# Performance work log

Hardware: AMD Instinct MI355X
Metric: run time of the kernel (lower is better)

## Reference

```python
import jax, jax.numpy as jnp
import numpy as np

IN_F = (16, 16, 16)
OUT_F = (16, 16, 16)
RANKS = (8, 8, 8, 8, 8, 8)


def setup_inputs() -> dict:
    key = jax.random.key(0)
    ks = jax.random.split(key, 9)
    x = jax.random.normal(ks[0], (4096, int(np.prod(IN_F))), dtype=jnp.float32)
    # core ~ U[0,1)*0.1 as in torch.rand(ranks)*0.1
    core = jax.random.uniform(ks[1], RANKS, dtype=jnp.float32) * 0.1
    # factor matrices: 3 out-side (out_f[i], r[i]) then 3 in-side (in_f[i], r[i+3])
    shapes = [(OUT_F[i], RANKS[i]) for i in range(3)] + [(IN_F[i], RANKS[i + 3]) for i in range(3)]
    f0, f1, f2, f3, f4, f5 = [
        jax.random.normal(ks[2 + i], shapes[i], dtype=jnp.float32) * 0.1 for i in range(6)
    ]
    bias = jnp.zeros((int(np.prod(OUT_F)),), dtype=jnp.float32)
    return {"x": x, "core": core, "f0": f0, "f1": f1, "f2": f2,
            "f3": f3, "f4": f4, "f5": f5, "bias": bias}


def reference(x, core, f0, f1, f2, f3, f4, f5, bias):
    # x: [N, prod(IN_F)] -> [N, i1, i2, i3]
    xr = x.reshape(-1, *IN_F)
    # Reconstruct full dense weight from Tucker factors (faithful to original)
    # core: [r0..r5]; f0..f2 out-side (out_dim, r); f3..f5 in-side (in_dim, r)
    W = jnp.einsum('ijklmn,ai,bj,ck,dl,em,fn->abcdef', core, f0, f1, f2, f3, f4, f5)
    # Contract input with in-side modes: [N, o1, o2, o3]
    res = jnp.einsum('abcdef,ndef->nabc', W, xr)
    y = res.reshape(-1, int(np.prod(OUT_F)))
    return y + bias
```

## Files before the change

### kernel.cpp

```cpp
#include <hip/hip_runtime.h>

#define THREADS 256

typedef __attribute__((ext_vector_type(8))) short bf16x8;
typedef __attribute__((ext_vector_type(4))) float f32x4;

__device__ inline unsigned short f2bf(float f) {
    union { float f; unsigned int u; } v; v.f = f;
    unsigned int r = v.u + 0x7fffu + ((v.u >> 16) & 1u);
    return (unsigned short)(r >> 16);
}

__global__ __launch_bounds__(THREADS) void k_in_contract(
    const float* __restrict__ x,
    const float* __restrict__ f3, const float* __restrict__ f4,
    const float* __restrict__ f5,
    unsigned short* __restrict__ u3b, int N)
{
    const int n = blockIdx.x;
    const int t = threadIdx.x;

    __shared__ float fs[256];
    __shared__ float u1s[256 * 9];
    __shared__ float u2s[128 * 9];

    if (t < 128) { fs[t] = f3[t]; fs[128 + t] = f4[t]; }

    float xv[16];
    {
        const float4* xr = (const float4*)(x + (size_t)n * 4096 + t * 16);
        float4 a0 = xr[0], a1 = xr[1], a2 = xr[2], a3 = xr[3];
        xv[0]=a0.x; xv[1]=a0.y; xv[2]=a0.z; xv[3]=a0.w;
        xv[4]=a1.x; xv[5]=a1.y; xv[6]=a1.z; xv[7]=a1.w;
        xv[8]=a2.x; xv[9]=a2.y; xv[10]=a2.z; xv[11]=a2.w;
        xv[12]=a3.x; xv[13]=a3.y; xv[14]=a3.z; xv[15]=a3.w;
    }

    float acc8[8];
    #pragma unroll
    for (int q = 0; q < 8; ++q) acc8[q] = 0.f;
    #pragma unroll
    for (int f = 0; f < 16; ++f) {
        const float xf = xv[f];
        #pragma unroll
        for (int n6 = 0; n6 < 8; ++n6)
            acc8[n6] = fmaf(xf, f5[f*8 + n6], acc8[n6]);
    }
    __syncthreads();
    #pragma unroll
    for (int n6 = 0; n6 < 8; ++n6) u1s[t*9 + n6] = acc8[n6];
    __syncthreads();

    {
        const int d = t >> 4, m = (t >> 1) & 7, h = t & 1;
        float fr[16];
        #pragma unroll
        for (int e = 0; e < 16; ++e) fr[e] = fs[128 + e*8 + m];
        float a4[4] = {0.f, 0.f, 0.f, 0.f};
        #pragma unroll
        for (int e = 0; e < 16; ++e) {
            const int base = (d*16 + e)*9 + h*4;
            #pragma unroll
            for (int q = 0; q < 4; ++q)
                a4[q] = fmaf(u1s[base + q], fr[e], a4[q]);
        }
        #pragma unroll
        for (int q = 0; q < 4; ++q) u2s[(d*8 + m)*9 + h*4 + q] = a4[q];
    }
    __syncthreads();

    {
        const int l = t >> 5, m = (t >> 2) & 7, h = t & 3;
        float fr[16];
        #pragma unroll
        for (int d = 0; d < 16; ++d) fr[d] = fs[d*8 + l];
        float a2[2] = {0.f, 0.f};
        #pragma unroll
        for (int d = 0; d < 16; ++d) {
            const int base = (d*8 + m)*9 + h*2;
            a2[0] = fmaf(u2s[base],     fr[d], a2[0]);
            a2[1] = fmaf(u2s[base + 1], fr[d], a2[1]);
        }
        unsigned int pk = (unsigned int)f2bf(a2[0]) |
                          ((unsigned int)f2bf(a2[1]) << 16);
        ((unsigned int*)u3b)[(size_t)n * 256 + t] = pk;
    }
}

__global__ __launch_bounds__(THREADS) void k_convert_core(
    const float* __restrict__ core, unsigned short* __restrict__ coreb)
{
    const int i = blockIdx.x * THREADS + threadIdx.x;
    float4 c = ((const float4*)core)[i];
    ushort4 o;
    o.x = f2bf(c.x); o.y = f2bf(c.y); o.z = f2bf(c.z); o.w = f2bf(c.w);
    ((ushort4*)coreb)[i] = o;
}

__global__ __launch_bounds__(THREADS) void k_core_gemm_mfma(
    const unsigned short* __restrict__ u3b,
    const unsigned short* __restrict__ coreb,
    float* __restrict__ v, int N)
{
    const int t    = threadIdx.x;
    const int lane = t & 63;
    const int wave = t >> 6;
    const int m0 = blockIdx.x * 128 + wave * 32;
    const int p0 = blockIdx.y * 32;
    const int lr = lane & 15;
    const int lq = lane >> 4;

    const unsigned short* aptr0 = u3b   + (size_t)(m0 + lr) * 512 + lq * 8;
    const unsigned short* aptr1 = aptr0 + 16 * 512;
    const unsigned short* bptr0 = coreb + (size_t)(p0 + lr) * 512 + lq * 8;
    const unsigned short* bptr1 = bptr0 + 16 * 512;

    f32x4 acc00 = {0.f,0.f,0.f,0.f}, acc01 = {0.f,0.f,0.f,0.f};
    f32x4 acc10 = {0.f,0.f,0.f,0.f}, acc11 = {0.f,0.f,0.f,0.f};

    #pragma unroll
    for (int k0 = 0; k0 < 512; k0 += 32) {
        bf16x8 a0 = *(const bf16x8*)(aptr0 + k0);
        bf16x8 a1 = *(const bf16x8*)(aptr1 + k0);
        bf16x8 b0 = *(const bf16x8*)(bptr0 + k0);
        bf16x8 b1 = *(const bf16x8*)(bptr1 + k0);
        acc00 = __builtin_amdgcn_mfma_f32_16x16x32_bf16(a0, b0, acc00, 0, 0, 0);
        acc01 = __builtin_amdgcn_mfma_f32_16x16x32_bf16(a0, b1, acc01, 0, 0, 0);
        acc10 = __builtin_amdgcn_mfma_f32_16x16x32_bf16(a1, b0, acc10, 0, 0, 0);
        acc11 = __builtin_amdgcn_mfma_f32_16x16x32_bf16(a1, b1, acc11, 0, 0, 0);
    }

    const int row = m0 + lq * 4;
    const int col = p0 + lr;
    #pragma unroll
    for (int r = 0; r < 4; ++r) {
        v[(size_t)(row + r) * 512 + col]           = acc00[r];
        v[(size_t)(row + r) * 512 + col + 16]      = acc01[r];
        v[(size_t)(row + 16 + r) * 512 + col]      = acc10[r];
        v[(size_t)(row + 16 + r) * 512 + col + 16] = acc11[r];
    }
}

__global__ __launch_bounds__(THREADS) void k_out_expand(
    const float* __restrict__ v,
    const float* __restrict__ f0, const float* __restrict__ f1,
    const float* __restrict__ f2, const float* __restrict__ bias,
    float* __restrict__ y, int N)
{
    const int n = blockIdx.x;
    const int t = threadIdx.x;

    __shared__ float fs[256];
    __shared__ float vs[512];
    __shared__ float w1s[128 * 9];
    __shared__ float w2s[256 * 9];

    if (t < 128) { fs[t] = f0[t]; fs[128 + t] = f1[t]; }
    if (t < 128) ((float4*)vs)[t] = ((const float4*)(v + (size_t)n*512))[t];
    __syncthreads();

    {
        const int a = t >> 4, j = (t >> 1) & 7, h = t & 1;
        float fr[8];
        #pragma unroll
        for (int i = 0; i < 8; ++i) fr[i] = fs[a*8 + i];
        float a4[4] = {0.f, 0.f, 0.f, 0.f};
        #pragma unroll
        for (int i = 0; i < 8; ++i) {
            const int base = i*64 + j*8 + h*4;
            #pragma unroll
            for (int q = 0; q < 4; ++q)
                a4[q] = fmaf(vs[base + q], fr[i], a4[q]);
        }
        #pragma unroll
        for (int q = 0; q < 4; ++q) w1s[(a*8 + j)*9 + h*4 + q] = a4[q];
    }
    __syncthreads();

    {
        const int a = t >> 4, b = t & 15;
        float fr[8];
        #pragma unroll
        for (int j = 0; j < 8; ++j) fr[j] = fs[128 + b*8 + j];
        float a8[8] = {0.f,0.f,0.f,0.f,0.f,0.f,0.f,0.f};
        #pragma unroll
        for (int j = 0; j < 8; ++j) {
            const int base = (a*8 + j)*9;
            const float fj = fr[j];
            #pragma unroll
            for (int k = 0; k < 8; ++k)
                a8[k] = fmaf(w1s[base + k], fj, a8[k]);
        }
        #pragma unroll
        for (int k = 0; k < 8; ++k) w2s[(a*16 + b)*9 + k] = a8[k];
    }
    __syncthreads();

    {
        const int a = t >> 4, b = t & 15;
        float wr[8];
        #pragma unroll
        for (int k = 0; k < 8; ++k) wr[k] = w2s[(a*16 + b)*9 + k];

        const int obase = a*256 + b*16;
        float4 b4[4];
        {
            const float4* bp = (const float4*)(bias + obase);
            b4[0] = bp[0]; b4[1] = bp[1]; b4[2] = bp[2]; b4[3] = bp[3];
        }
        float yv[16];
        #pragma unroll
        for (int q = 0; q < 4; ++q) {
            yv[q*4+0] = b4[q].x; yv[q*4+1] = b4[q].y;
            yv[q*4+2] = b4[q].z; yv[q*4+3] = b4[q].w;
        }
        #pragma unroll
        for (int c = 0; c < 16; ++c) {
            float s = yv[c];
            #pragma unroll
            for (int k = 0; k < 8; ++k)
                s = fmaf(wr[k], f2[c*8 + k], s);
            yv[c] = s;
        }
        float4* o = (float4*)(y + (size_t)n*4096 + obase);
        #pragma unroll
        for (int q = 0; q < 4; ++q)
            o[q] = make_float4(yv[q*4+0], yv[q*4+1], yv[q*4+2], yv[q*4+3]);
    }
}

extern "C" void kernel_launch(void* const* d_in, const int* in_sizes, int n_in,
                              void* d_out, int out_size, void* d_ws, size_t ws_size,
                              hipStream_t stream)
{
    const float* x    = (const float*)d_in[0];
    const float* core = (const float*)d_in[1];
    const float* f0   = (const float*)d_in[2];
    const float* f1   = (const float*)d_in[3];
    const float* f2   = (const float*)d_in[4];
    const float* f3   = (const float*)d_in[5];
    const float* f4   = (const float*)d_in[6];
    const float* f5   = (const float*)d_in[7];
    const float* bias = (const float*)d_in[8];
    float* y = (float*)d_out;

    const int N = in_sizes[0] / 4096;

    unsigned short* u3b   = (unsigned short*)d_ws;
    unsigned short* coreb = u3b + (size_t)N * 512;
    float*          v     = (float*)(coreb + 512 * 512);

    k_in_contract<<<N, THREADS, 0, stream>>>(x, f3, f4, f5, u3b, N);
    k_convert_core<<<256, THREADS, 0, stream>>>(core, coreb);
    dim3 gb(N / 128, 512 / 32);
    k_core_gemm_mfma<<<gb, THREADS, 0, stream>>>(u3b, coreb, v, N);
    k_out_expand<<<N, THREADS, 0, stream>>>(v, f0, f1, f2, bias, y, N);
}
```

Baseline: 163.5 us.

## Fuse core GEMM with output expansion and fold core conversion into input contraction

Cuts the pipeline from four launches to two. The core bf16 conversion moves into the input-contraction kernel, which now handles two rows per block. The MFMA core GEMM is fused with the three output-side factor contractions, so each block computes 8 rows of v in shared memory and expands them directly to y. This drops the v round-trip through global memory and two launches. In exchange, the fused GEMM uses only 8 of the 16 MFMA rows and each block rereads the whole core matrix, and intermediates are now stored as bf16, which lowers precision.

```diff
diff --git a/kernel.cpp b/kernel.cpp
--- a/kernel.cpp
+++ b/kernel.cpp
@@ -10,45 +10,69 @@
     unsigned int r = v.u + 0x7fffu + ((v.u >> 16) & 1u);
     return (unsigned short)(r >> 16);
 }
-
-__global__ __launch_bounds__(THREADS) void k_in_contract(
+__device__ inline unsigned int pack2(float lo, float hi) {
+    return (unsigned int)f2bf(lo) | ((unsigned int)f2bf(hi) << 16);
+}
+__device__ inline float bflo(unsigned int u) {
+    union { unsigned int u; float f; } v; v.u = u << 16; return v.f;
+}
+__device__ inline float bfhi(unsigned int u) {
+    union { unsigned int u; float f; } v; v.u = u & 0xffff0000u; return v.f;
+}
+
+__global__ __launch_bounds__(THREADS) void k_in_contract2(
     const float* __restrict__ x,
     const float* __restrict__ f3, const float* __restrict__ f4,
-    const float* __restrict__ f5,
-    unsigned short* __restrict__ u3b, int N)
+    const float* __restrict__ f5, const float* __restrict__ core,
+    unsigned short* __restrict__ u3b, unsigned short* __restrict__ coreb,
+    int N)
 {
-    const int n = blockIdx.x;
-    const int t = threadIdx.x;
+    const int n0 = blockIdx.x * 2;
+    const int t  = threadIdx.x;
 
     __shared__ float fs[256];
-    __shared__ float u1s[256 * 9];
-    __shared__ float u2s[128 * 9];
+    __shared__ float u1s[2][256 * 9];
+    __shared__ float u2s[2][128 * 9];
 
     if (t < 128) { fs[t] = f3[t]; fs[128 + t] = f4[t]; }
 
-    float xv[16];
-    {
-        const float4* xr = (const float4*)(x + (size_t)n * 4096 + t * 16);
+    if (blockIdx.x < 256) {
+        const int i = blockIdx.x * THREADS + t;
+        float4 c = ((const float4*)core)[i];
+        ushort4 o;
+        o.x = f2bf(c.x); o.y = f2bf(c.y); o.z = f2bf(c.z); o.w = f2bf(c.w);
+        ((ushort4*)coreb)[i] = o;
+    }
+
+    float xv[2][16];
+    #pragma unroll
+    for (int rr = 0; rr < 2; ++rr) {
+        const float4* xr = (const float4*)(x + (size_t)(n0 + rr) * 4096 + t * 16);
         float4 a0 = xr[0], a1 = xr[1], a2 = xr[2], a3 = xr[3];
-        xv[0]=a0.x; xv[1]=a0.y; xv[2]=a0.z; xv[3]=a0.w;
-        xv[4]=a1.x; xv[5]=a1.y; xv[6]=a1.z; xv[7]=a1.w;
-        xv[8]=a2.x; xv[9]=a2.y; xv[10]=a2.z; xv[11]=a2.w;
-        xv[12]=a3.x; xv[13]=a3.y; xv[14]=a3.z; xv[15]=a3.w;
-    }
-
-    float acc8[8];
-    #pragma unroll
-    for (int q = 0; q < 8; ++q) acc8[q] = 0.f;
+        xv[rr][0]=a0.x;  xv[rr][1]=a0.y;  xv[rr][2]=a0.z;  xv[rr][3]=a0.w;
+        xv[rr][4]=a1.x;  xv[rr][5]=a1.y;  xv[rr][6]=a1.z;  xv[rr][7]=a1.w;
+        xv[rr][8]=a2.x;  xv[rr][9]=a2.y;  xv[rr][10]=a2.z; xv[rr][11]=a2.w;
+        xv[rr][12]=a3.x; xv[rr][13]=a3.y; xv[rr][14]=a3.z; xv[rr][15]=a3.w;
+    }
+
+    float acc8[2][8];
+    #pragma unroll
+    for (int q = 0; q < 8; ++q) { acc8[0][q] = 0.f; acc8[1][q] = 0.f; }
     #pragma unroll
     for (int f = 0; f < 16; ++f) {
-        const float xf = xv[f];
-        #pragma unroll
-        for (int n6 = 0; n6 < 8; ++n6)
-            acc8[n6] = fmaf(xf, f5[f*8 + n6], acc8[n6]);
-    }
-    __syncthreads();
-    #pragma unroll
-    for (int n6 = 0; n6 < 8; ++n6) u1s[t*9 + n6] = acc8[n6];
+        #pragma unroll
+        for (int n6 = 0; n6 < 8; ++n6) {
+            const float w = f5[f*8 + n6];
+            acc8[0][n6] = fmaf(xv[0][f], w, acc8[0][n6]);
+            acc8[1][n6] = fmaf(xv[1][f], w, acc8[1][n6]);
+        }
+    }
+    __syncthreads();
+    #pragma unroll
+    for (int n6 = 0; n6 < 8; ++n6) {
+        u1s[0][t*9 + n6] = acc8[0][n6];
+        u1s[1][t*9 + n6] = acc8[1][n6];
+    }
     __syncthreads();
 
     {
@@ -56,16 +80,21 @@
         float fr[16];
         #pragma unroll
         for (int e = 0; e < 16; ++e) fr[e] = fs[128 + e*8 + m];
-        float a4[4] = {0.f, 0.f, 0.f, 0.f};
+        float a4[2][4] = {};
         #pragma unroll
         for (int e = 0; e < 16; ++e) {
             const int base = (d*16 + e)*9 + h*4;
             #pragma unroll
-            for (int q = 0; q < 4; ++q)
-                a4[q] = fmaf(u1s[base + q], fr[e], a4[q]);
-        }
-        #pragma unroll
-        for (int q = 0; q < 4; ++q) u2s[(d*8 + m)*9 + h*4 + q] = a4[q];
+            for (int q = 0; q < 4; ++q) {
+                a4[0][q] = fmaf(u1s[0][base + q], fr[e], a4[0][q]);
+                a4[1][q] = fmaf(u1s[1][base + q], fr[e], a4[1][q]);
+            }
+        }
+        #pragma unroll
+        for (int q = 0; q < 4; ++q) {
+            u2s[0][(d*8 + m)*9 + h*4 + q] = a4[0][q];
+            u2s[1][(d*8 + m)*9 + h*4 + q] = a4[1][q];
+        }
     }
     __syncthreads();
 
@@ -74,158 +103,154 @@
         float fr[16];
         #pragma unroll
         for (int d = 0; d < 16; ++d) fr[d] = fs[d*8 + l];
-        float a2[2] = {0.f, 0.f};
+        float a2[2][2] = {};
         #pragma unroll
         for (int d = 0; d < 16; ++d) {
             const int base = (d*8 + m)*9 + h*2;
-            a2[0] = fmaf(u2s[base],     fr[d], a2[0]);
-            a2[1] = fmaf(u2s[base + 1], fr[d], a2[1]);
-        }
-        unsigned int pk = (unsigned int)f2bf(a2[0]) |
-                          ((unsigned int)f2bf(a2[1]) << 16);
-        ((unsigned int*)u3b)[(size_t)n * 256 + t] = pk;
-    }
-}
-
-__global__ __launch_bounds__(THREADS) void k_convert_core(
-    const float* __restrict__ core, unsigned short* __restrict__ coreb)
-{
-    const int i = blockIdx.x * THREADS + threadIdx.x;
-    float4 c = ((const float4*)core)[i];
-    ushort4 o;
-    o.x = f2bf(c.x); o.y = f2bf(c.y); o.z = f2bf(c.z); o.w = f2bf(c.w);
-    ((ushort4*)coreb)[i] = o;
-}
-
-__global__ __launch_bounds__(THREADS) void k_core_gemm_mfma(
+            a2[0][0] = fmaf(u2s[0][base],     fr[d], a2[0][0]);
+            a2[0][1] = fmaf(u2s[0][base + 1], fr[d], a2[0][1]);
+            a2[1][0] = fmaf(u2s[1][base],     fr[d], a2[1][0]);
+            a2[1][1] = fmaf(u2s[1][base + 1], fr[d], a2[1][1]);
+        }
+        ((unsigned int*)u3b)[(size_t)(n0+0) * 256 + t] = pack2(a2[0][0], a2[0][1]);
+        ((unsigned int*)u3b)[(size_t)(n0+1) * 256 + t] = pack2(a2[1][0], a2[1][1]);
+    }
+}
+
+__global__ __launch_bounds__(THREADS) void k_gemm_expand(
     const unsigned short* __restrict__ u3b,
     const unsigned short* __restrict__ coreb,
-    float* __restrict__ v, int N)
-{
-    const int t    = threadIdx.x;
-    const int lane = t & 63;
-    const int wave = t >> 6;
-    const int m0 = blockIdx.x * 128 + wave * 32;
-    const int p0 = blockIdx.y * 32;
-    const int lr = lane & 15;
-    const int lq = lane >> 4;
-
-    const unsigned short* aptr0 = u3b   + (size_t)(m0 + lr) * 512 + lq * 8;
-    const unsigned short* aptr1 = aptr0 + 16 * 512;
-    const unsigned short* bptr0 = coreb + (size_t)(p0 + lr) * 512 + lq * 8;
-    const unsigned short* bptr1 = bptr0 + 16 * 512;
-
-    f32x4 acc00 = {0.f,0.f,0.f,0.f}, acc01 = {0.f,0.f,0.f,0.f};
-    f32x4 acc10 = {0.f,0.f,0.f,0.f}, acc11 = {0.f,0.f,0.f,0.f};
-
-    #pragma unroll
-    for (int k0 = 0; k0 < 512; k0 += 32) {
-        bf16x8 a0 = *(const bf16x8*)(aptr0 + k0);
-        bf16x8 a1 = *(const bf16x8*)(aptr1 + k0);
-        bf16x8 b0 = *(const bf16x8*)(bptr0 + k0);
-        bf16x8 b1 = *(const bf16x8*)(bptr1 + k0);
-        acc00 = __builtin_amdgcn_mfma_f32_16x16x32_bf16(a0, b0, acc00, 0, 0, 0);
-        acc01 = __builtin_amdgcn_mfma_f32_16x16x32_bf16(a0, b1, acc01, 0, 0, 0);
-        acc10 = __builtin_amdgcn_mfma_f32_16x16x32_bf16(a1, b0, acc10, 0, 0, 0);
-        acc11 = __builtin_amdgcn_mfma_f32_16x16x32_bf16(a1, b1, acc11, 0, 0, 0);
-    }
-
-    const int row = m0 + lq * 4;
-    const int col = p0 + lr;
-    #pragma unroll
-    for (int r = 0; r < 4; ++r) {
-        v[(size_t)(row + r) * 512 + col]           = acc00[r];
-        v[(size_t)(row + r) * 512 + col + 16]      = acc01[r];
-        v[(size_t)(row + 16 + r) * 512 + col]      = acc10[r];
-        v[(size_t)(row + 16 + r) * 512 + col + 16] = acc11[r];
-    }
-}
-
-__global__ __launch_bounds__(THREADS) void k_out_expand(
-    const float* __restrict__ v,
     const float* __restrict__ f0, const float* __restrict__ f1,
     const float* __restrict__ f2, const float* __restrict__ bias,
     float* __restrict__ y, int N)
 {
-    const int n = blockIdx.x;
-    const int t = threadIdx.x;
-
-    __shared__ float fs[256];
-    __shared__ float vs[512];
-    __shared__ float w1s[128 * 9];
-    __shared__ float w2s[256 * 9];
-
-    if (t < 128) { fs[t] = f0[t]; fs[128 + t] = f1[t]; }
-    if (t < 128) ((float4*)vs)[t] = ((const float4*)(v + (size_t)n*512))[t];
-    __syncthreads();
-
-    {
-        const int a = t >> 4, j = (t >> 1) & 7, h = t & 1;
-        float fr[8];
-        #pragma unroll
-        for (int i = 0; i < 8; ++i) fr[i] = fs[a*8 + i];
-        float a4[4] = {0.f, 0.f, 0.f, 0.f};
-        #pragma unroll
-        for (int i = 0; i < 8; ++i) {
-            const int base = i*64 + j*8 + h*4;
-            #pragma unroll
-            for (int q = 0; q < 4; ++q)
-                a4[q] = fmaf(vs[base + q], fr[i], a4[q]);
-        }
-        #pragma unroll
-        for (int q = 0; q < 4; ++q) w1s[(a*8 + j)*9 + h*4 + q] = a4[q];
-    }
-    __syncthreads();
-
-    {
-        const int a = t >> 4, b = t & 15;
-        float fr[8];
-        #pragma unroll
-        for (int j = 0; j < 8; ++j) fr[j] = fs[128 + b*8 + j];
-        float a8[8] = {0.f,0.f,0.f,0.f,0.f,0.f,0.f,0.f};
+    __shared__ float        vsS[8 * 520];
+    __shared__ unsigned int w1S[8 * 528];
+    __shared__ unsigned int w2S[8 * 1300];
+    __shared__ float        fsS[256];
+
+    const int t  = threadIdx.x;
+    const int r0 = blockIdx.x * 8;
+
+    fsS[t] = (t < 128) ? f0[t] : f1[t - 128];
+
+    {
+        const int lane = t & 63, w = t >> 6;
+        const int lr = lane & 15, lq = lane >> 4;
+        const unsigned short* ap = u3b + (size_t)(r0 + (lr & 7)) * 512 + lq * 8;
+        const unsigned short* bp = coreb + (size_t)(w * 128 + lr) * 512 + lq * 8;
+
+        f32x4 acc[8];
+        #pragma unroll
+        for (int c = 0; c < 8; ++c) acc[c] = (f32x4){0.f, 0.f, 0.f, 0.f};
+
+        #pragma unroll
+        for (int k0 = 0; k0 < 512; k0 += 32) {
+            bf16x8 a = *(const bf16x8*)(ap + k0);
+            #pragma unroll
+            for (int c = 0; c < 8; ++c) {
+                bf16x8 b = *(const bf16x8*)(bp + c * 8192 + k0);
+                acc[c] = __builtin_amdgcn_mfma_f32_16x16x32_bf16(a, b, acc[c], 0, 0, 0);
+            }
+        }
+        if (lq < 2) {
+            #pragma unroll
+            for (int c = 0; c < 8; ++c)
+                #pragma unroll
+                for (int q = 0; q < 4; ++q)
+                    vsS[(lq*4 + q)*520 + w*128 + c*16 + lr] = acc[c][q];
+        }
+    }
+    __syncthreads();
+
+    {
+        const int r = t >> 5, a = (t >> 1) & 15, h = t & 1;
+        const float* vrow = vsS + r*520 + h*32;
+        float fa[8];
+        #pragma unroll
+        for (int i = 0; i < 8; ++i) fa[i] = fsS[a*8 + i];
+        #pragma unroll
+        for (int q2 = 0; q2 < 16; ++q2) {
+            float s0 = 0.f, s1 = 0.f;
+            #pragma unroll
+            for (int i = 0; i < 8; ++i) {
+                s0 = fmaf(fa[i], vrow[i*64 + 2*q2],     s0);
+                s1 = fmaf(fa[i], vrow[i*64 + 2*q2 + 1], s1);
+            }
+            w1S[r*528 + a*33 + h*16 + q2] = pack2(s0, s1);
+        }
+    }
+    __syncthreads();
+
+    {
+        const int r = t >> 5, a = (t >> 1) & 15, h = t & 1;
+        const unsigned int* w1row = w1S + r*528 + a*33;
+        float acc[8][8] = {};
         #pragma unroll
         for (int j = 0; j < 8; ++j) {
-            const int base = (a*8 + j)*9;
-            const float fj = fr[j];
+            float wj[8];
+            #pragma unroll
+            for (int k2 = 0; k2 < 4; ++k2) {
+                const unsigned int u = w1row[j*4 + k2];
+                wj[2*k2]     = bflo(u);
+                wj[2*k2 + 1] = bfhi(u);
+            }
+            #pragma unroll
+            for (int bi = 0; bi < 8; ++bi) {
+                const float fb = fsS[128 + (h*8 + bi)*8 + j];
+                #pragma unroll
+                for (int k = 0; k < 8; ++k)
+                    acc[bi][k] = fmaf(fb, wj[k], acc[bi][k]);
+            }
+        }
+        #pragma unroll
+        for (int bi = 0; bi < 8; ++bi) {
+            const int b = h*8 + bi;
+            #pragma unroll
+            for (int k2 = 0; k2 < 4; ++k2)
+                w2S[r*1300 + a*5 + b*81 + k2] = pack2(acc[bi][2*k2], acc[bi][2*k2+1]);
+        }
+    }
+    __syncthreads();
+
+    {
+        const int cq = t & 3, s = t >> 2;
+        float f2r[4][8];
+        #pragma unroll
+        for (int cc = 0; cc < 4; ++cc)
             #pragma unroll
             for (int k = 0; k < 8; ++k)
-                a8[k] = fmaf(w1s[base + k], fj, a8[k]);
-        }
-        #pragma unroll
-        for (int k = 0; k < 8; ++k) w2s[(a*16 + b)*9 + k] = a8[k];
-    }
-    __syncthreads();
-
-    {
-        const int a = t >> 4, b = t & 15;
-        float wr[8];
-        #pragma unroll
-        for (int k = 0; k < 8; ++k) wr[k] = w2s[(a*16 + b)*9 + k];
-
-        const int obase = a*256 + b*16;
-        float4 b4[4];
-        {
-            const float4* bp = (const float4*)(bias + obase);
-            b4[0] = bp[0]; b4[1] = bp[1]; b4[2] = bp[2]; b4[3] = bp[3];
-        }
-        float yv[16];
-        #pragma unroll
-        for (int q = 0; q < 4; ++q) {
-            yv[q*4+0] = b4[q].x; yv[q*4+1] = b4[q].y;
-            yv[q*4+2] = b4[q].z; yv[q*4+3] = b4[q].w;
-        }
-        #pragma unroll
-        for (int c = 0; c < 16; ++c) {
-            float s = yv[c];
-            #pragma unroll
-            for (int k = 0; k < 8; ++k)
-                s = fmaf(wr[k], f2[c*8 + k], s);
-            yv[c] = s;
-        }
-        float4* o = (float4*)(y + (size_t)n*4096 + obase);
-        #pragma unroll
-        for (int q = 0; q < 4; ++q)
-            o[q] = make_float4(yv[q*4+0], yv[q*4+1], yv[q*4+2], yv[q*4+3]);
+                f2r[cc][k] = f2[(cq*4 + cc)*8 + k];
+        float4 br[4];
+        #pragma unroll
+        for (int g = 0; g < 4; ++g)
+            br[g] = *(const float4*)(bias + (size_t)(s + 64*g)*16 + cq*4);
+
+        #pragma unroll
+        for (int r = 0; r < 8; ++r) {
+            float4* orow = (float4*)(y + (size_t)(r0 + r) * 4096);
+            #pragma unroll
+            for (int g = 0; g < 4; ++g) {
+                const int ab = s + 64*g, a = ab >> 4, b = ab & 15;
+                const unsigned int* w2row = w2S + r*1300 + a*5 + b*81;
+                float wf[8];
+                #pragma unroll
+                for (int k2 = 0; k2 < 4; ++k2) {
+                    const unsigned int u = w2row[k2];
+                    wf[2*k2]     = bflo(u);
+                    wf[2*k2 + 1] = bfhi(u);
+                }
+                float4 o = br[g];
+                #pragma unroll
+                for (int k = 0; k < 8; ++k) {
+                    o.x = fmaf(f2r[0][k], wf[k], o.x);
+                    o.y = fmaf(f2r[1][k], wf[k], o.y);
+                    o.z = fmaf(f2r[2][k], wf[k], o.z);
+                    o.w = fmaf(f2r[3][k], wf[k], o.w);
+                }
+                orow[t + 256*g] = o;
+            }
+        }
     }
 }
 
@@ -248,11 +273,7 @@
 
     unsigned short* u3b   = (unsigned short*)d_ws;
     unsigned short* coreb = u3b + (size_t)N * 512;
-    float*          v     = (float*)(coreb + 512 * 512);
-
-    k_in_contract<<<N, THREADS, 0, stream>>>(x, f3, f4, f5, u3b, N);
-    k_convert_core<<<256, THREADS, 0, stream>>>(core, coreb);
-    dim3 gb(N / 128, 512 / 32);
-    k_core_gemm_mfma<<<gb, THREADS, 0, stream>>>(u3b, coreb, v, N);
-    k_out_expand<<<N, THREADS, 0, stream>>>(v, f0, f1, f2, bias, y, N);
-}
+
+    k_in_contract2<<<N / 2, THREADS, 0, stream>>>(x, f3, f4, f5, core, u3b, coreb, N);
+    k_gemm_expand<<<N / 8, THREADS, 0, stream>>>(u3b, coreb, f0, f1, f2, bias, y, N);
+}
```

After: 166.7 us. About the same (+1.9%).

## Fuse core conversion into input contraction, process two rows per block, retile GEMM

Applied to the files above, without the earlier changes.

Folds the core-to-bf16 conversion into the input contraction kernel, which removes one kernel launch. That kernel now handles two samples per block and reuses the factor loads and shared-memory setup for both. The core GEMM is retiled so each wave computes a 32x16 output tile and each block covers 64x32, which doubles the grid to raise occupancy but gives less register reuse per wave. The two-row kernel doubles its shared memory use, which may lower occupancy.

```diff
diff --git a/kernel.cpp b/kernel.cpp
--- a/kernel.cpp
+++ b/kernel.cpp
@@ -10,45 +10,63 @@
     unsigned int r = v.u + 0x7fffu + ((v.u >> 16) & 1u);
     return (unsigned short)(r >> 16);
 }
-
-__global__ __launch_bounds__(THREADS) void k_in_contract(
+__device__ inline unsigned int pack2(float lo, float hi) {
+    return (unsigned int)f2bf(lo) | ((unsigned int)f2bf(hi) << 16);
+}
+
+__global__ __launch_bounds__(THREADS) void k_in_contract2(
     const float* __restrict__ x,
     const float* __restrict__ f3, const float* __restrict__ f4,
-    const float* __restrict__ f5,
-    unsigned short* __restrict__ u3b, int N)
-{
-    const int n = blockIdx.x;
-    const int t = threadIdx.x;
+    const float* __restrict__ f5, const float* __restrict__ core,
+    unsigned short* __restrict__ u3b, unsigned short* __restrict__ coreb,
+    int N)
+{
+    const int n0 = blockIdx.x * 2;
+    const int t  = threadIdx.x;
 
     __shared__ float fs[256];
-    __shared__ float u1s[256 * 9];
-    __shared__ float u2s[128 * 9];
+    __shared__ float u1s[2][256 * 9];
+    __shared__ float u2s[2][128 * 9];
 
     if (t < 128) { fs[t] = f3[t]; fs[128 + t] = f4[t]; }
 
-    float xv[16];
-    {
-        const float4* xr = (const float4*)(x + (size_t)n * 4096 + t * 16);
+    if (blockIdx.x < 256) {
+        const int i = blockIdx.x * THREADS + t;
+        float4 c = ((const float4*)core)[i];
+        ushort4 o;
+        o.x = f2bf(c.x); o.y = f2bf(c.y); o.z = f2bf(c.z); o.w = f2bf(c.w);
+        ((ushort4*)coreb)[i] = o;
+    }
+
+    float xv[2][16];
+    #pragma unroll
+    for (int rr = 0; rr < 2; ++rr) {
+        const float4* xr = (const float4*)(x + (size_t)(n0 + rr) * 4096 + t * 16);
         float4 a0 = xr[0], a1 = xr[1], a2 = xr[2], a3 = xr[3];
-        xv[0]=a0.x; xv[1]=a0.y; xv[2]=a0.z; xv[3]=a0.w;
-        xv[4]=a1.x; xv[5]=a1.y; xv[6]=a1.z; xv[7]=a1.w;
-        xv[8]=a2.x; xv[9]=a2.y; xv[10]=a2.z; xv[11]=a2.w;
-        xv[12]=a3.x; xv[13]=a3.y; xv[14]=a3.z; xv[15]=a3.w;
-    }
-
-    float acc8[8];
-    #pragma unroll
-    for (int q = 0; q < 8; ++q) acc8[q] = 0.f;
+        xv[rr][0]=a0.x;  xv[rr][1]=a0.y;  xv[rr][2]=a0.z;  xv[rr][3]=a0.w;
+        xv[rr][4]=a1.x;  xv[rr][5]=a1.y;  xv[rr][6]=a1.z;  xv[rr][7]=a1.w;
+        xv[rr][8]=a2.x;  xv[rr][9]=a2.y;  xv[rr][10]=a2.z; xv[rr][11]=a2.w;
+        xv[rr][12]=a3.x; xv[rr][13]=a3.y; xv[rr][14]=a3.z; xv[rr][15]=a3.w;
+    }
+
+    float acc8[2][8];
+    #pragma unroll
+    for (int q = 0; q < 8; ++q) { acc8[0][q] = 0.f; acc8[1][q] = 0.f; }
     #pragma unroll
     for (int f = 0; f < 16; ++f) {
-        const float xf = xv[f];
-        #pragma unroll
-        for (int n6 = 0; n6 < 8; ++n6)
-            acc8[n6] = fmaf(xf, f5[f*8 + n6], acc8[n6]);
-    }
-    __syncthreads();
-    #pragma unroll
-    for (int n6 = 0; n6 < 8; ++n6) u1s[t*9 + n6] = acc8[n6];
+        #pragma unroll
+        for (int n6 = 0; n6 < 8; ++n6) {
+            const float w = f5[f*8 + n6];
+            acc8[0][n6] = fmaf(xv[0][f], w, acc8[0][n6]);
+            acc8[1][n6] = fmaf(xv[1][f], w, acc8[1][n6]);
+        }
+    }
+    __syncthreads();
+    #pragma unroll
+    for (int n6 = 0; n6 < 8; ++n6) {
+        u1s[0][t*9 + n6] = acc8[0][n6];
+        u1s[1][t*9 + n6] = acc8[1][n6];
+    }
     __syncthreads();
 
     {
@@ -56,16 +74,21 @@
         float fr[16];
         #pragma unroll
         for (int e = 0; e < 16; ++e) fr[e] = fs[128 + e*8 + m];
-        float a4[4] = {0.f, 0.f, 0.f, 0.f};
+        float a4[2][4] = {};
         #pragma unroll
         for (int e = 0; e < 16; ++e) {
             const int base = (d*16 + e)*9 + h*4;
             #pragma unroll
-            for (int q = 0; q < 4; ++q)
-                a4[q] = fmaf(u1s[base + q], fr[e], a4[q]);
-        }
-        #pragma unroll
-        for (int q = 0; q < 4; ++q) u2s[(d*8 + m)*9 + h*4 + q] = a4[q];
+            for (int q = 0; q < 4; ++q) {
+                a4[0][q] = fmaf(u1s[0][base + q], fr[e], a4[0][q]);
+                a4[1][q] = fmaf(u1s[1][base + q], fr[e], a4[1][q]);
+            }
+        }
+        #pragma unroll
+        for (int q = 0; q < 4; ++q) {
+            u2s[0][(d*8 + m)*9 + h*4 + q] = a4[0][q];
+            u2s[1][(d*8 + m)*9 + h*4 + q] = a4[1][q];
+        }
     }
     __syncthreads();
 
@@ -74,70 +97,48 @@
         float fr[16];
         #pragma unroll
         for (int d = 0; d < 16; ++d) fr[d] = fs[d*8 + l];
-        float a2[2] = {0.f, 0.f};
+        float a2[2][2] = {};
         #pragma unroll
         for (int d = 0; d < 16; ++d) {
             const int base = (d*8 + m)*9 + h*2;
-            a2[0] = fmaf(u2s[base],     fr[d], a2[0]);
-            a2[1] = fmaf(u2s[base + 1], fr[d], a2[1]);
-        }
-        unsigned int pk = (unsigned int)f2bf(a2[0]) |
-                          ((unsigned int)f2bf(a2[1]) << 16);
-        ((unsigned int*)u3b)[(size_t)n * 256 + t] = pk;
-    }
-}
-
-__global__ __launch_bounds__(THREADS) void k_convert_core(
-    const float* __restrict__ core, unsigned short* __restrict__ coreb)
-{
-    const int i = blockIdx.x * THREADS + threadIdx.x;
-    float4 c = ((const float4*)core)[i];
-    ushort4 o;
-    o.x = f2bf(c.x); o.y = f2bf(c.y); o.z = f2bf(c.z); o.w = f2bf(c.w);
-    ((ushort4*)coreb)[i] = o;
-}
-
-__global__ __launch_bounds__(THREADS) void k_core_gemm_mfma(
+            a2[0][0] = fmaf(u2s[0][base],     fr[d], a2[0][0]);
+            a2[0][1] = fmaf(u2s[0][base + 1], fr[d], a2[0][1]);
+            a2[1][0] = fmaf(u2s[1][base],     fr[d], a2[1][0]);
+            a2[1][1] = fmaf(u2s[1][base + 1], fr[d], a2[1][1]);
+        }
+        ((unsigned int*)u3b)[(size_t)(n0+0) * 256 + t] = pack2(a2[0][0], a2[0][1]);
+        ((unsigned int*)u3b)[(size_t)(n0+1) * 256 + t] = pack2(a2[1][0], a2[1][1]);
+    }
+}
+
+__global__ __launch_bounds__(THREADS) void k_b(
     const unsigned short* __restrict__ u3b,
     const unsigned short* __restrict__ coreb,
-    float* __restrict__ v, int N)
-{
-    const int t    = threadIdx.x;
-    const int lane = t & 63;
-    const int wave = t >> 6;
-    const int m0 = blockIdx.x * 128 + wave * 32;
-    const int p0 = blockIdx.y * 32;
-    const int lr = lane & 15;
-    const int lq = lane >> 4;
-
-    const unsigned short* aptr0 = u3b   + (size_t)(m0 + lr) * 512 + lq * 8;
-    const unsigned short* aptr1 = aptr0 + 16 * 512;
-    const unsigned short* bptr0 = coreb + (size_t)(p0 + lr) * 512 + lq * 8;
-    const unsigned short* bptr1 = bptr0 + 16 * 512;
-
-    f32x4 acc00 = {0.f,0.f,0.f,0.f}, acc01 = {0.f,0.f,0.f,0.f};
-    f32x4 acc10 = {0.f,0.f,0.f,0.f}, acc11 = {0.f,0.f,0.f,0.f};
-
+    float* __restrict__ v)
+{
+    const int t = threadIdx.x, lane = t & 63, w = t >> 6;
+    const int m0 = blockIdx.x * 64 + (w >> 1) * 32;
+    const int p0 = blockIdx.y * 32 + (w & 1) * 16;
+    const int lr = lane & 15, lq = lane >> 4;
+
+    const unsigned short* ap0 = u3b + (size_t)(m0 + lr) * 512 + lq * 8;
+    const unsigned short* ap1 = ap0 + 16 * 512;
+    const unsigned short* bp  = coreb + (size_t)(p0 + lr) * 512 + lq * 8;
+
+    f32x4 acc0 = {0.f,0.f,0.f,0.f}, acc1 = {0.f,0.f,0.f,0.f};
     #pragma unroll
     for (int k0 = 0; k0 < 512; k0 += 32) {
-        bf16x8 a0 = *(const bf16x8*)(aptr0 + k0);
-        bf16x8 a1 = *(const bf16x8*)(aptr1 + k0);
-        bf16x8 b0 = *(const bf16x8*)(bptr0 + k0);
-        bf16x8 b1 = *(const bf16x8*)(bptr1 + k0);
-        acc00 = __builtin_amdgcn_mfma_f32_16x16x32_bf16(a0, b0, acc00, 0, 0, 0);
-        acc01 = __builtin_amdgcn_mfma_f32_16x16x32_bf16(a0, b1, acc01, 0, 0, 0);
-        acc10 = __builtin_amdgcn_mfma_f32_16x16x32_bf16(a1, b0, acc10, 0, 0, 0);
-        acc11 = __builtin_amdgcn_mfma_f32_16x16x32_bf16(a1, b1, acc11, 0, 0, 0);
-    }
-
-    const int row = m0 + lq * 4;
-    const int col = p0 + lr;
-    #pragma unroll
-    for (int r = 0; r < 4; ++r) {
-        v[(size_t)(row + r) * 512 + col]           = acc00[r];
-        v[(size_t)(row + r) * 512 + col + 16]      = acc01[r];
-        v[(size_t)(row + 16 + r) * 512 + col]      = acc10[r];
-        v[(size_t)(row + 16 + r) * 512 + col + 16] = acc11[r];
+        bf16x8 a0 = *(const bf16x8*)(ap0 + k0);
+        bf16x8 a1 = *(const bf16x8*)(ap1 + k0);
+        bf16x8 b  = *(const bf16x8*)(bp  + k0);
+        acc0 = __builtin_amdgcn_mfma_f32_16x16x32_bf16(a0, b, acc0, 0, 0, 0);
+        acc1 = __builtin_amdgcn_mfma_f32_16x16x32_bf16(a1, b, acc1, 0, 0, 0);
+    }
+    const int col = p0 + lr, row = m0 + lq * 4;
+    #pragma unroll
+    for (int q = 0; q < 4; ++q) {
+        v[(size_t)(row + q) * 512 + col]      = acc0[q];
+        v[(size_t)(row + 16 + q) * 512 + col] = acc1[q];
     }
 }
 
@@ -250,9 +251,8 @@
     unsigned short* coreb = u3b + (size_t)N * 512;
     float*          v     = (float*)(coreb + 512 * 512);
 
-    k_in_contract<<<N, THREADS, 0, stream>>>(x, f3, f4, f5, u3b, N);
-    k_convert_core<<<256, THREADS, 0, stream>>>(core, coreb);
-    dim3 gb(N / 128, 512 / 32);
-    k_core_gemm_mfma<<<gb, THREADS, 0, stream>>>(u3b, coreb, v, N);
+    k_in_contract2<<<N / 2, THREADS, 0, stream>>>(x, f3, f4, f5, core, u3b, coreb, N);
+    dim3 gb(N / 64, 16);
+    k_b<<<gb, THREADS, 0, stream>>>(u3b, coreb, v);
     k_out_expand<<<N, THREADS, 0, stream>>>(v, f0, f1, f2, bias, y, N);
 }
```

Result: slower. 169.0 us (+3.3%).
